# Performance work log

Measured on AMD Instinct MI355X. Metric: run time of the kernel, lower is better.

## Reference

```python
import jax, jax.numpy as jnp
import numpy as np

B = 32768
H = 320          # pred_hidden
V = 34           # num_classes
BLANK = V - 1    # padding_idx for embedding


def setup_inputs() -> dict:
    key = jax.random.key(0)
    ks = jax.random.split(key, 12)
    s = 0.05
    embed_W = jax.random.normal(ks[0], (V, H), jnp.float32) * s
    embed_W = embed_W.at[BLANK].set(0.0)  # padding_idx row is zeros in torch
    return {
        "x": jax.random.randint(ks[1], (B,), 0, V, jnp.int32),
        "enc_proj_line": jax.random.normal(ks[2], (B, H), jnp.float32),
        "h": jax.random.normal(ks[3], (1, B, H), jnp.float32),
        "c": jax.random.normal(ks[4], (1, B, H), jnp.float32),
        "embed_W": embed_W,
        "W_ih": jax.random.normal(ks[5], (4 * H, H), jnp.float32) * s,
        "W_hh": jax.random.normal(ks[6], (4 * H, H), jnp.float32) * s,
        "b_ih": jax.random.normal(ks[7], (4 * H,), jnp.float32) * s,
        "b_hh": jax.random.normal(ks[8], (4 * H,), jnp.float32) * s,
        "pred_W": jax.random.normal(ks[9], (H, H), jnp.float32) * s,
        "pred_b": jnp.zeros((H,), jnp.float32),
        "joint_W": jax.random.normal(ks[10], (V, H), jnp.float32) * s,
        "joint_b": jnp.zeros((V,), jnp.float32),
    }


def reference(x, enc_proj_line, h, c, embed_W, W_ih, W_hh, b_ih, b_hh,
              pred_W, pred_b, joint_W, joint_b):
    # embedding lookup: [B, H]
    emb = embed_W[x]
    # single-timestep LSTM cell (torch gate order: i, f, g, o)
    gates = emb @ W_ih.T + b_ih + h[0] @ W_hh.T + b_hh  # [B, 4H]
    i, f, g, o = jnp.split(gates, 4, axis=-1)
    i = jax.nn.sigmoid(i)
    f = jax.nn.sigmoid(f)
    g = jnp.tanh(g)
    o = jax.nn.sigmoid(o)
    c_new = f * c[0] + i * g                 # [B, H]
    h_new = o * jnp.tanh(c_new)              # [B, H] == g[0] (lstm output)
    # pred projection + joint
    pred_proj = h_new @ pred_W.T + pred_b    # [B, H]
    joint_out = (enc_proj_line + pred_proj) @ joint_W.T + joint_b  # [B, V]
    dec = jnp.argmax(joint_out, axis=-1)
    return dec, h_new[None], c_new[None]
```

## Files before the change

### kernel.cpp

```cpp
#include <hip/hip_runtime.h>
#include <math.h>

#define NB 32768
#define H 320
#define V 34
#define N4 1280
#define BM 128
#define BN 128
#define BK 32
#define KSTEPS (H / BK)
#define NWG ((NB / BM) * (N4 / BN))

typedef _Float16 f16;
typedef f16 f16x4 __attribute__((ext_vector_type(4)));
typedef f16 f16x8 __attribute__((ext_vector_type(8)));
typedef float f32x4 __attribute__((ext_vector_type(4)));

#define WS_GTP 0
#define WS_JB2 54400
#define WS_B_BYTE 217744
#define BT_COUNT (N4 * H)
#define WS_JP_BYTE 1856144
#define JP_COUNT (48 * 640)
#define WS_AT_BYTE 1979136
#define AT_COUNT (NB * H)

#define JBM 64
#define JBK 32
#define JKSTEPS 20

#define PREP_P4 1280
#define PREP_P2 50
#define PREP_P0 170
#define PREP_P3 120
#define PREP_NWG (PREP_P4 + PREP_P2 + PREP_P0 + PREP_P3 + 1)

__device__ __forceinline__ float sigf(float x) {
    return 1.0f / (1.0f + __expf(-x));
}
__device__ __forceinline__ float tanh_fast(float x) {
    return 1.0f - 2.0f / (1.0f + __expf(2.0f * x));
}

typedef const __attribute__((address_space(1))) unsigned int* gas_t;
typedef __attribute__((address_space(3))) unsigned int* las_t;

__device__ __forceinline__ void split8(const float* e, f16x8& p1, f16x8& p2) {
    #pragma unroll
    for (int j = 0; j < 8; ++j) {
        f16 a = (f16)e[j];
        p1[j] = a;
        p2[j] = (f16)((e[j] - (float)a) * 2048.0f);
    }
}

__global__ void prep(const float* __restrict__ embed_W,
                     const float* __restrict__ W_ih,
                     const float* __restrict__ b_ih,
                     const float* __restrict__ b_hh,
                     const float* __restrict__ pred_W,
                     const float* __restrict__ pred_b,
                     const float* __restrict__ joint_W,
                     const float* __restrict__ joint_b,
                     const float* __restrict__ W_hh,
                     const float* __restrict__ h_in,
                     float* __restrict__ ws) {
    const int bid = blockIdx.x;
    const int t = threadIdx.x;
    if (bid < PREP_P4) {
        int id = bid * 256 + t;
        int ks = id >> 15, m = id & 32767;
        const float* src = h_in + (size_t)m * H + ks * 32;
        f16* at1 = (f16*)((char*)ws + WS_AT_BYTE);
        f16* at2 = at1 + AT_COUNT;
        size_t tbase = ((size_t)(m >> 7) * KSTEPS + ks) * 4096
                       + ((m & 127) >> 4) * 512 + (m & 15) * 8;
        #pragma unroll
        for (int g = 0; g < 4; ++g) {
            float4 v0 = *(const float4*)(src + g * 8);
            float4 v1 = *(const float4*)(src + g * 8 + 4);
            float e[8] = {v0.x, v0.y, v0.z, v0.w, v1.x, v1.y, v1.z, v1.w};
            f16x8 p1, p2;
            split8(e, p1, p2);
            *(f16x8*)(at1 + tbase + g * 128) = p1;
            *(f16x8*)(at2 + tbase + g * 128) = p2;
        }
    } else if (bid < PREP_P4 + PREP_P2) {
        int id = (bid - PREP_P4) * 256 + t;
        int ks = id / 1280, n = id - ks * 1280;
        int orig = (n & 3) * H + (n >> 2);
        const float* src = W_hh + (size_t)orig * H + ks * 32;
        f16* bt1 = (f16*)((char*)ws + WS_B_BYTE);
        f16* bt2 = bt1 + BT_COUNT;
        size_t tbase = ((size_t)(n >> 7) * KSTEPS + ks) * 4096
                       + ((n & 127) >> 4) * 512 + (n & 15) * 8;
        #pragma unroll
        for (int g = 0; g < 4; ++g) {
            float4 v0 = *(const float4*)(src + g * 8);
            float4 v1 = *(const float4*)(src + g * 8 + 4);
            float e[8] = {v0.x, v0.y, v0.z, v0.w, v1.x, v1.y, v1.z, v1.w};
            f16x8 p1, p2;
            split8(e, p1, p2);
            *(f16x8*)(bt1 + tbase + g * 128) = p1;
            *(f16x8*)(bt2 + tbase + g * 128) = p2;
        }
    } else if (bid < PREP_P4 + PREP_P2 + PREP_P0) {
        int id = (bid - PREP_P4 - PREP_P2) * 256 + t;
        int v = id / N4, n = id % N4;
        int orig = (n & 3) * H + (n >> 2);
        float acc = b_ih[orig] + b_hh[orig];
        const float* e = embed_W + (size_t)v * H;
        const float* w = W_ih + (size_t)orig * H;
        for (int k = 0; k < H; k += 4) {
            float4 e4 = *(const float4*)(e + k);
            float4 w4 = *(const float4*)(w + k);
            acc = fmaf(e4.x, w4.x, acc);
            acc = fmaf(e4.y, w4.y, acc);
            acc = fmaf(e4.z, w4.z, acc);
            acc = fmaf(e4.w, w4.w, acc);
        }
        ws[WS_GTP + id] = acc;
    } else if (bid < PREP_P4 + PREP_P2 + PREP_P0 + PREP_P3) {
        int id = (bid - PREP_P4 - PREP_P2 - PREP_P0) * 256 + t;
        int n = id / 640, k = id % 640;
        float wv = 0.0f;
        if (n < V) {
            if (k < H) {
                wv = joint_W[(size_t)n * H + k];
            } else {
                float acc = 0.0f;
                const float* jw = joint_W + (size_t)n * H;
                for (int j = 0; j < H; ++j)
                    acc = fmaf(jw[j], pred_W[(size_t)j * H + (k - H)], acc);
                wv = acc;
            }
        }
        f16 w1 = (f16)wv;
        f16 w2 = (f16)((wv - (float)w1) * 2048.0f);
        int kk = k & 31;
        int off = (k >> 5) * 1536 + (n >> 4) * 512 + (kk >> 3) * 128
                  + (n & 15) * 8 + (kk & 7);
        f16* jp1 = (f16*)((char*)ws + WS_JP_BYTE);
        jp1[off] = w1;
        jp1[JP_COUNT + off] = w2;
    } else {
        if (t < V) {
            float acc = joint_b[t];
            const float* jw = joint_W + (size_t)t * H;
            for (int j = 0; j < H; ++j)
                acc = fmaf(jw[j], pred_b[j], acc);
            ws[WS_JB2 + t] = acc;
        }
    }
}

__launch_bounds__(256, 2)
__global__ void lstm_gemm_fast(const int* __restrict__ x,
                               const float* __restrict__ c_in,
                               const float* __restrict__ ws,
                               float* __restrict__ out) {
    __shared__ __align__(16) char smem[65536];
    const int tid = threadIdx.x, lane = tid & 63, w = tid >> 6;

    int l = (blockIdx.x & 7) * (NWG / 8) + (blockIdx.x >> 3);
    const int mb = l / (N4 / BN);
    const int nb = l % (N4 / BN);
    const int m0 = mb * BM, n0 = nb * BN;

    const f16* At1 = (const f16*)((const char*)ws + WS_AT_BYTE);
    const f16* Bt1 = (const f16*)((const char*)ws + WS_B_BYTE);
    const float* gtp = ws + WS_GTP;
    float* hn_out = out + NB;
    float* cn_out = out + NB + (size_t)NB * H;

    f32x4 accM[4][4], accC[4][4];
    #pragma unroll
    for (int i = 0; i < 4; ++i)
        #pragma unroll
        for (int j = 0; j < 4; ++j) {
            accM[i][j] = (f32x4){0.f, 0.f, 0.f, 0.f};
            accC[i][j] = (f32x4){0.f, 0.f, 0.f, 0.f};
        }

    auto stage = [&](int ks, int buf) {
        const f16* src;
        if (w == 0)      src = At1 + (size_t)(mb * KSTEPS + ks) * 4096;
        else if (w == 1) src = At1 + AT_COUNT + (size_t)(mb * KSTEPS + ks) * 4096;
        else if (w == 2) src = Bt1 + (size_t)(nb * KSTEPS + ks) * 4096;
        else             src = Bt1 + BT_COUNT + (size_t)(nb * KSTEPS + ks) * 4096;
        char* ldst = smem + buf * 32768 + w * 8192;
        #pragma unroll
        for (int i = 0; i < 8; ++i) {
            __builtin_amdgcn_global_load_lds(
                (gas_t)(const void*)(src + i * 512 + lane * 8),
                (las_t)(void*)(ldst + i * 1024), 16, 0, 0);
        }
    };

    stage(0, 0);
    __syncthreads();

    const int asub = (w >> 1) * 4;
    const int bsub = (w & 1) * 4;
    const int lo = lane * 8;
    int cur = 0;
    for (int t = 0; t < KSTEPS; ++t) {
        if (t < KSTEPS - 1) stage(t + 1, cur ^ 1);
        const f16* A1 = (const f16*)(smem + cur * 32768);
        const f16* A2 = A1 + 4096;
        const f16* B1 = A1 + 8192;
        const f16* B2 = A1 + 12288;

        f16x8 a[4], b1[4], b2[4];
        #pragma unroll
        for (int mi = 0; mi < 4; ++mi)
            a[mi] = *(const f16x8*)(A1 + (asub + mi) * 512 + lo);
        #pragma unroll
        for (int nj = 0; nj < 4; ++nj)
            b1[nj] = *(const f16x8*)(B1 + (bsub + nj) * 512 + lo);
        #pragma unroll
        for (int mi = 0; mi < 4; ++mi)
            #pragma unroll
            for (int nj = 0; nj < 4; ++nj)
                accM[mi][nj] = __builtin_amdgcn_mfma_f32_16x16x32_f16(
                    a[mi], b1[nj], accM[mi][nj], 0, 0, 0);
        #pragma unroll
        for (int nj = 0; nj < 4; ++nj)
            b2[nj] = *(const f16x8*)(B2 + (bsub + nj) * 512 + lo);
        #pragma unroll
        for (int mi = 0; mi < 4; ++mi)
            #pragma unroll
            for (int nj = 0; nj < 4; ++nj)
                accC[mi][nj] = __builtin_amdgcn_mfma_f32_16x16x32_f16(
                    a[mi], b2[nj], accC[mi][nj], 0, 0, 0);
        #pragma unroll
        for (int mi = 0; mi < 4; ++mi)
            a[mi] = *(const f16x8*)(A2 + (asub + mi) * 512 + lo);
        #pragma unroll
        for (int mi = 0; mi < 4; ++mi)
            #pragma unroll
            for (int nj = 0; nj < 4; ++nj)
                accC[mi][nj] = __builtin_amdgcn_mfma_f32_16x16x32_f16(
                    a[mi], b1[nj], accC[mi][nj], 0, 0, 0);
        __syncthreads();
        cur ^= 1;
    }

    const int wm = (w >> 1) * 64, wn = (w & 1) * 64;
    float* gates = (float*)smem;
    #pragma unroll
    for (int mi = 0; mi < 4; ++mi)
        #pragma unroll
        for (int nj = 0; nj < 4; ++nj) {
            f32x4 vm = accM[mi][nj];
            f32x4 vc = accC[mi][nj];
            int n = wn + nj * 16 + (lane & 15);
            int mb4 = wm + mi * 16 + (lane >> 4) * 4;
            #pragma unroll
            for (int q = 0; q < 4; ++q) {
                int row = mb4 + q;
                gates[row * 128 + (n ^ ((row & 7) << 2))] =
                    fmaf(vc[q], 1.0f / 2048.0f, vm[q]);
            }
        }
    __syncthreads();

    const int hk0 = n0 >> 2;
    #pragma unroll 4
    for (int it = 0; it < 16; ++it) {
        int idx = it * 256 + tid;
        int ml = idx >> 5, hkl = idx & 31;
        int k0 = (ml & 7) << 2;
        f32x4 g4 = *(const f32x4*)&gates[ml * 128 + ((hkl * 4) ^ k0)];
        int m = m0 + ml;
        int hk = hk0 + hkl;
        int xv = x[m];
        float4 b4 = *(const float4*)(gtp + (size_t)xv * N4 + n0 + hkl * 4);
        float ig = sigf(g4[0] + b4.x);
        float fg = sigf(g4[1] + b4.y);
        float gg = tanh_fast(g4[2] + b4.z);
        float og = sigf(g4[3] + b4.w);
        float cv = c_in[(size_t)m * H + hk];
        float cn = fmaf(fg, cv, ig * gg);
        float hn = og * tanh_fast(cn);
        hn_out[(size_t)m * H + hk] = hn;
        cn_out[(size_t)m * H + hk] = cn;
    }
}

__launch_bounds__(256, 2)
__global__ void joint_argmax(const float* __restrict__ enc,
                             const float* __restrict__ ws,
                             float* __restrict__ out) {
    __shared__ __align__(16) char smem[28672];
    const int tid = threadIdx.x, lane = tid & 63, w = tid >> 6;
    const int m0 = blockIdx.x * JBM;

    const f16* Jp1 = (const f16*)((const char*)ws + WS_JP_BYTE);
    const f16* Jp2 = Jp1 + JP_COUNT;
    const float* hn = out + NB;
    const float* jb2 = ws + WS_JB2;

    f16* base = (f16*)smem;

    f32x4 accM[3], accC[3];
    #pragma unroll
    for (int j = 0; j < 3; ++j) {
        accM[j] = (f32x4){0.f, 0.f, 0.f, 0.f};
        accC[j] = (f32x4){0.f, 0.f, 0.f, 0.f};
    }

    auto stage = [&](int t, f16* A1, f16* A2, f16* B1, f16* B2) {
        const float* srcp = (t < 10) ? enc : hn;
        const int koff = (t % 10) * JBK;
        int row = (tid >> 6) * 16 + (tid & 15);
        int k0 = ((tid & 63) >> 4) * 8;
        const float* sp = srcp + (size_t)(m0 + row) * H + koff + k0;
        float4 v0 = *(const float4*)sp;
        float4 v1 = *(const float4*)(sp + 4);
        float e[8] = {v0.x, v0.y, v0.z, v0.w, v1.x, v1.y, v1.z, v1.w};
        f16x8 p1, p2;
        split8(e, p1, p2);
        *(f16x8*)(A1 + tid * 8) = p1;
        *(f16x8*)(A2 + tid * 8) = p2;
        if (tid < 192) {
            *(int4*)(B1 + tid * 8) = *(const int4*)(Jp1 + t * 1536 + tid * 8);
            *(int4*)(B2 + tid * 8) = *(const int4*)(Jp2 + t * 1536 + tid * 8);
        }
    };

    stage(0, base, base + 2048, base + 4096, base + 5632);
    __syncthreads();

    const int lo = lane * 8;
    int cur = 0;
    for (int t = 0; t < JKSTEPS; ++t) {
        if (t < JKSTEPS - 1) {
            f16* nb_ = base + (cur ^ 1) * 7168;
            stage(t + 1, nb_, nb_ + 2048, nb_ + 4096, nb_ + 5632);
        }
        f16* A1 = base + cur * 7168;
        f16* A2 = A1 + 2048;
        f16* B1 = A1 + 4096;
        f16* B2 = A1 + 5632;

        f16x8 a1 = *(const f16x8*)(A1 + w * 512 + lo);
        f16x8 a2 = *(const f16x8*)(A2 + w * 512 + lo);
        f16x8 b1[3], b2[3];
        #pragma unroll
        for (int nj = 0; nj < 3; ++nj) {
            b1[nj] = *(const f16x8*)(B1 + nj * 512 + lo);
            b2[nj] = *(const f16x8*)(B2 + nj * 512 + lo);
        }
        #pragma unroll
        for (int nj = 0; nj < 3; ++nj) {
            accM[nj] = __builtin_amdgcn_mfma_f32_16x16x32_f16(a1, b1[nj], accM[nj], 0, 0, 0);
            accC[nj] = __builtin_amdgcn_mfma_f32_16x16x32_f16(a1, b2[nj], accC[nj], 0, 0, 0);
            accC[nj] = __builtin_amdgcn_mfma_f32_16x16x32_f16(a2, b1[nj], accC[nj], 0, 0, 0);
        }
        __syncthreads();
        cur ^= 1;
    }

    float* lg = (float*)smem;
    const int wm = w * 16;
    #pragma unroll
    for (int nj = 0; nj < 3; ++nj) {
        int n = nj * 16 + (lane & 15);
        int mr = wm + (lane >> 4) * 4;
        #pragma unroll
        for (int q = 0; q < 4; ++q)
            lg[(mr + q) * 49 + n] = fmaf(accC[nj][q], 1.0f / 2048.0f, accM[nj][q]);
    }
    __syncthreads();

    if (tid < JBM) {
        const float* row = lg + tid * 49;
        float best = row[0] + jb2[0];
        int bi = 0;
        #pragma unroll
        for (int v = 1; v < V; ++v) {
            float t2 = row[v] + jb2[v];
            if (t2 > best) { best = t2; bi = v; }
        }
        out[m0 + tid] = (float)bi;
    }
}

extern "C" void kernel_launch(void* const* d_in, const int* in_sizes, int n_in,
                              void* d_out, int out_size, void* d_ws, size_t ws_size,
                              hipStream_t stream) {
    const int*   x       = (const int*)  d_in[0];
    const float* enc     = (const float*)d_in[1];
    const float* h       = (const float*)d_in[2];
    const float* c       = (const float*)d_in[3];
    const float* embed_W = (const float*)d_in[4];
    const float* W_ih    = (const float*)d_in[5];
    const float* W_hh    = (const float*)d_in[6];
    const float* b_ih    = (const float*)d_in[7];
    const float* b_hh    = (const float*)d_in[8];
    const float* pred_W  = (const float*)d_in[9];
    const float* pred_b  = (const float*)d_in[10];
    const float* joint_W = (const float*)d_in[11];
    const float* joint_b = (const float*)d_in[12];
    float* out = (float*)d_out;
    float* ws  = (float*)d_ws;

    prep<<<PREP_NWG, 256, 0, stream>>>(embed_W, W_ih, b_ih, b_hh,
                                       pred_W, pred_b, joint_W, joint_b,
                                       W_hh, h, ws);
    lstm_gemm_fast<<<NWG, 256, 0, stream>>>(x, c, ws, out);
    joint_argmax<<<NB / JBM, 256, 0, stream>>>(enc, ws, out);
}
```

Baseline: 163.3 us.

## Load A fragments directly to registers, stage only B via LDS

The A operand (hi and lo f16 splits) is now read straight from global memory into registers, prefetched one k-step ahead. Only the B operands go through LDS, which halves the LDS staging footprint per buffer and spreads the B loads across all four waves. Manual vmcnt waits, sched_barriers and s_setprio around the MFMA blocks are added to control overlap. The cost is more registers for the double-buffered A fragments and the fully unrolled loop, plus reliance on exact vmcnt accounting for correctness.

```diff
diff --git a/kernel.cpp b/kernel.cpp
--- a/kernel.cpp
+++ b/kernel.cpp
@@ -168,11 +168,29 @@
     const int m0 = mb * BM, n0 = nb * BN;
 
     const f16* At1 = (const f16*)((const char*)ws + WS_AT_BYTE);
+    const f16* At2 = At1 + AT_COUNT;
     const f16* Bt1 = (const f16*)((const char*)ws + WS_B_BYTE);
+    const f16* Bt2 = Bt1 + BT_COUNT;
     const float* gtp = ws + WS_GTP;
     float* hn_out = out + NB;
     float* cn_out = out + NB + (size_t)NB * H;
 
+    const int asub = (w >> 1) * 4;
+    const int bsub = (w & 1) * 4;
+    const int lo = lane * 8;
+
+    auto stageB = [&](int ks, int parity) {
+        const f16* srcp = (w < 2) ? Bt1 : Bt2;
+        const f16* src = srcp + (size_t)(nb * KSTEPS + ks) * 4096 + (w & 1) * 2048;
+        char* dst = smem + parity * 16384 + (w >> 1) * 8192 + (w & 1) * 4096;
+        #pragma unroll
+        for (int i = 0; i < 4; ++i) {
+            __builtin_amdgcn_global_load_lds(
+                (gas_t)(const void*)(src + i * 512 + lane * 8),
+                (las_t)(void*)(dst + i * 1024), 16, 0, 0);
+        }
+    };
+
     f32x4 accM[4][4], accC[4][4];
     #pragma unroll
     for (int i = 0; i < 4; ++i)
@@ -182,68 +200,79 @@
             accC[i][j] = (f32x4){0.f, 0.f, 0.f, 0.f};
         }
 
-    auto stage = [&](int ks, int buf) {
-        const f16* src;
-        if (w == 0)      src = At1 + (size_t)(mb * KSTEPS + ks) * 4096;
-        else if (w == 1) src = At1 + AT_COUNT + (size_t)(mb * KSTEPS + ks) * 4096;
-        else if (w == 2) src = Bt1 + (size_t)(nb * KSTEPS + ks) * 4096;
-        else             src = Bt1 + BT_COUNT + (size_t)(nb * KSTEPS + ks) * 4096;
-        char* ldst = smem + buf * 32768 + w * 8192;
-        #pragma unroll
-        for (int i = 0; i < 8; ++i) {
-            __builtin_amdgcn_global_load_lds(
-                (gas_t)(const void*)(src + i * 512 + lane * 8),
-                (las_t)(void*)(ldst + i * 1024), 16, 0, 0);
-        }
-    };
-
-    stage(0, 0);
-    __syncthreads();
-
-    const int asub = (w >> 1) * 4;
-    const int bsub = (w & 1) * 4;
-    const int lo = lane * 8;
-    int cur = 0;
+    f16x8 a1r[2][4], a2r[4], b1[4], b2[4];
+
+    stageB(0, 0);
+    __builtin_amdgcn_sched_barrier(0);
+    {
+        const f16* a1b = At1 + (size_t)(mb * KSTEPS + 0) * 4096;
+        #pragma unroll
+        for (int mi = 0; mi < 4; ++mi)
+            a1r[0][mi] = *(const f16x8*)(a1b + (asub + mi) * 512 + lo);
+    }
+    asm volatile("s_waitcnt vmcnt(4)" ::: "memory");
+    __builtin_amdgcn_sched_barrier(0);
+    __builtin_amdgcn_s_barrier();
+
+    #pragma unroll
     for (int t = 0; t < KSTEPS; ++t) {
-        if (t < KSTEPS - 1) stage(t + 1, cur ^ 1);
-        const f16* A1 = (const f16*)(smem + cur * 32768);
-        const f16* A2 = A1 + 4096;
-        const f16* B1 = A1 + 8192;
-        const f16* B2 = A1 + 12288;
-
-        f16x8 a[4], b1[4], b2[4];
-        #pragma unroll
-        for (int mi = 0; mi < 4; ++mi)
-            a[mi] = *(const f16x8*)(A1 + (asub + mi) * 512 + lo);
+        const int cb = t & 1;
+        {
+            const f16* a2b = At2 + (size_t)(mb * KSTEPS + t) * 4096;
+            #pragma unroll
+            for (int mi = 0; mi < 4; ++mi)
+                a2r[mi] = *(const f16x8*)(a2b + (asub + mi) * 512 + lo);
+        }
+        __builtin_amdgcn_sched_barrier(0);
+        if (t < KSTEPS - 1) {
+            stageB(t + 1, cb ^ 1);
+            __builtin_amdgcn_sched_barrier(0);
+            const f16* a1b = At1 + (size_t)(mb * KSTEPS + (t + 1)) * 4096;
+            #pragma unroll
+            for (int mi = 0; mi < 4; ++mi)
+                a1r[cb ^ 1][mi] = *(const f16x8*)(a1b + (asub + mi) * 512 + lo);
+            __builtin_amdgcn_sched_barrier(0);
+        }
+
+        const f16* B1 = (const f16*)(smem + cb * 16384);
+        const f16* B2 = B1 + 4096;
+
         #pragma unroll
         for (int nj = 0; nj < 4; ++nj)
             b1[nj] = *(const f16x8*)(B1 + (bsub + nj) * 512 + lo);
+        __builtin_amdgcn_s_setprio(1);
         #pragma unroll
         for (int mi = 0; mi < 4; ++mi)
             #pragma unroll
             for (int nj = 0; nj < 4; ++nj)
                 accM[mi][nj] = __builtin_amdgcn_mfma_f32_16x16x32_f16(
-                    a[mi], b1[nj], accM[mi][nj], 0, 0, 0);
+                    a1r[cb][mi], b1[nj], accM[mi][nj], 0, 0, 0);
+        __builtin_amdgcn_s_setprio(0);
         #pragma unroll
         for (int nj = 0; nj < 4; ++nj)
             b2[nj] = *(const f16x8*)(B2 + (bsub + nj) * 512 + lo);
+        __builtin_amdgcn_s_setprio(1);
         #pragma unroll
         for (int mi = 0; mi < 4; ++mi)
             #pragma unroll
             for (int nj = 0; nj < 4; ++nj)
                 accC[mi][nj] = __builtin_amdgcn_mfma_f32_16x16x32_f16(
-                    a[mi], b2[nj], accC[mi][nj], 0, 0, 0);
-        #pragma unroll
-        for (int mi = 0; mi < 4; ++mi)
-            a[mi] = *(const f16x8*)(A2 + (asub + mi) * 512 + lo);
+                    a1r[cb][mi], b2[nj], accC[mi][nj], 0, 0, 0);
         #pragma unroll
         for (int mi = 0; mi < 4; ++mi)
             #pragma unroll
             for (int nj = 0; nj < 4; ++nj)
                 accC[mi][nj] = __builtin_amdgcn_mfma_f32_16x16x32_f16(
-                    a[mi], b1[nj], accC[mi][nj], 0, 0, 0);
-        __syncthreads();
-        cur ^= 1;
+                    a2r[mi], b1[nj], accC[mi][nj], 0, 0, 0);
+        __builtin_amdgcn_s_setprio(0);
+
+        if (t < KSTEPS - 1) {
+            asm volatile("s_waitcnt vmcnt(4)" ::: "memory");
+            __builtin_amdgcn_sched_barrier(0);
+            __builtin_amdgcn_s_barrier();
+        } else {
+            __syncthreads();
+        }
     }
 
     const int wm = (w >> 1) * 64, wn = (w & 1) * 64;
```

Measured after the change: 162.5 us. Within noise of the previous version (-0.5%).
